# Kernel tuning notes

Hardware: AMD Instinct MI355X
Metric: run time of the kernel (lower is better)

The kernel has to match this reference:

```python
import jax, jax.numpy as jnp
import numpy as np

C_IN, C_OUT, N_FILTERS = 64, 256, 16
CK = C_IN * N_FILTERS  # 1024
B, N, E = 2, 10000, 120000


def setup_inputs() -> dict:
    key = jax.random.key(0)
    k1, k2, k3, k4, k5, k6, k7, k8 = jax.random.split(key, 8)
    node_feats = jax.random.normal(k1, (B, N, C_IN), dtype=jnp.float32)
    node_positions = jax.random.uniform(k2, (B, N, 3), dtype=jnp.float32)
    edge_src = jax.random.randint(k3, (E,), 0, N, dtype=jnp.int32)
    edge_dst = jax.random.randint(k4, (E,), 0, N, dtype=jnp.int32)
    # original skips self-connections inside the adjacency list (self term is added separately)
    edge_src = jnp.where(edge_src == edge_dst, (edge_src + 1) % N, edge_src)
    W_dir = jax.random.normal(k5, (CK, 3), dtype=jnp.float32) * 0.05
    b_dir = jax.random.normal(k6, (CK,), dtype=jnp.float32) * 0.05
    W_feat = jax.random.normal(k7, (C_OUT, CK), dtype=jnp.float32) * 0.05
    b_feat = jax.random.normal(k8, (C_OUT,), dtype=jnp.float32) * 0.05
    return {"node_feats": node_feats, "node_positions": node_positions,
            "edge_src": edge_src, "edge_dst": edge_dst,
            "W_dir": W_dir, "b_dir": b_dir, "W_feat": W_feat, "b_feat": b_feat}


def reference(node_feats, node_positions, edge_src, edge_dst, W_dir, b_dir, W_feat, b_feat):
    n = node_feats.shape[1]
    # stacked features: node_feats repeated n_filters times along channels -> [B,N,CK]
    stacked = jnp.tile(node_feats, (1, 1, N_FILTERS))
    # per-edge direction: pos_other - pos_this  (this = dst node being aggregated into)
    d = node_positions[:, edge_src] - node_positions[:, edge_dst]  # [B,E,3]
    aff = jax.nn.relu(jnp.einsum('bed,kd->bek', d, W_dir) + b_dir)  # [B,E,CK]
    msg = stacked[:, edge_src] * aff                                 # [B,E,CK]
    agg = jax.vmap(lambda m: jax.ops.segment_sum(m, edge_dst, num_segments=n))(msg)  # [B,N,CK]
    # self contribution: direction = 0 -> relu(b_dir), gated own features
    agg = agg + stacked * jax.nn.relu(b_dir)
    out = jax.nn.relu(jnp.einsum('bnk,ok->bno', agg, W_feat) + b_feat)  # [B,N,c_out]
    return out
```

## Files before the change

kernel.cpp:

```cpp
#include <hip/hip_runtime.h>
#include <hip/hip_bf16.h>
#include <cstdint>
#include <cstddef>

constexpr int BATCH = 2;
constexpr int C_IN  = 64;
constexpr int CK    = 1024;
constexpr int C_OUT = 256;

using bf16x8 = __attribute__((ext_vector_type(8))) short;
using f32x4  = __attribute__((ext_vector_type(4))) float;

#define GLOAD_LDS16(g, s) \
    __builtin_amdgcn_global_load_lds((const __attribute__((address_space(1))) void*)(g), \
                                     (__attribute__((address_space(3))) void*)(s), 16, 0, 0)

__global__ void hist_kernel(const int* __restrict__ dst, int* __restrict__ counts, int E) {
    int e = blockIdx.x * blockDim.x + threadIdx.x;
    if (e < E) atomicAdd(&counts[dst[e]], 1);
}

__global__ __launch_bounds__(1024)
void scan_kernel(const int* __restrict__ counts, int* __restrict__ offsets, int n) {
    __shared__ int wsum[16];
    __shared__ int carry_s;
    const int t = threadIdx.x;
    const int lane = t & 63;
    const int w = t >> 6;
    if (t == 0) carry_s = 0;
    __syncthreads();
    const int nch = (n + 1023) >> 10;
    for (int c = 0; c < nch; ++c) {
        const int idx = (c << 10) + t;
        const int v = (idx < n) ? counts[idx] : 0;
        int x = v;
        #pragma unroll
        for (int off = 1; off < 64; off <<= 1) {
            int y = __shfl_up(x, off, 64);
            if (lane >= off) x += y;
        }
        if (lane == 63) wsum[w] = x;
        __syncthreads();
        int wpre = 0, total = 0;
        #pragma unroll
        for (int i = 0; i < 16; ++i) {
            const int s = wsum[i];
            if (i < w) wpre += s;
            total += s;
        }
        const int carry = carry_s;
        if (idx < n) offsets[idx] = carry + wpre + (x - v);
        __syncthreads();
        if (t == 0) carry_s = carry + total;
    }
    if (t == 0) offsets[n] = carry_s;
}

__global__ void scatter_kernel(const int* __restrict__ dst, const int* __restrict__ src,
                               const int* __restrict__ offsets,
                               int* __restrict__ cursors, int* __restrict__ sorted_src, int E) {
    int e = blockIdx.x * blockDim.x + threadIdx.x;
    if (e < E) {
        const int d = dst[e];
        const int p = atomicAdd(&cursors[d], 1);
        sorted_src[offsets[d] + p] = src[e];
    }
}

__global__ __launch_bounds__(256)
void agg_kernel(const float* __restrict__ feats, const float* __restrict__ pos,
                const int* __restrict__ sorted_src, const int* __restrict__ offsets,
                const float* __restrict__ W_dir, const float* __restrict__ b_dir,
                __hip_bfloat16* __restrict__ agg, int N) {
    const int n = blockIdx.x;
    const int b = blockIdx.y;
    const int t = threadIdx.x;
    const int c0 = (2 * t) & 63;
    const float* posb   = pos   + (size_t)b * N * 3;
    const float* featsb = feats + (size_t)b * N * C_IN;

    const float px = posb[n * 3 + 0];
    const float py = posb[n * 3 + 1];
    const float pz = posb[n * 3 + 2];

    float wx[4], wy[4], wz[4], bb[4];
    #pragma unroll
    for (int u = 0; u < 4; ++u) {
        const int k = 2 * t + 512 * (u >> 1) + (u & 1);
        wx[u] = W_dir[k * 3 + 0];
        wy[u] = W_dir[k * 3 + 1];
        wz[u] = W_dir[k * 3 + 2];
        bb[u] = b_dir[k];
    }

    float acc[4] = {0.f, 0.f, 0.f, 0.f};
    const int beg = offsets[n];
    const int end = offsets[n + 1];
    for (int j = beg; j < end; ++j) {
        const int s = sorted_src[j];
        const float dx = posb[s * 3 + 0] - px;
        const float dy = posb[s * 3 + 1] - py;
        const float dz = posb[s * 3 + 2] - pz;
        const float2 f = *reinterpret_cast<const float2*>(featsb + (size_t)s * C_IN + c0);
        #pragma unroll
        for (int u = 0; u < 4; ++u) {
            const float a = fmaxf(fmaf(dx, wx[u], fmaf(dy, wy[u], fmaf(dz, wz[u], bb[u]))), 0.f);
            acc[u] += ((u & 1) ? f.y : f.x) * a;
        }
    }
    const float2 fs = *reinterpret_cast<const float2*>(featsb + (size_t)n * C_IN + c0);
    #pragma unroll
    for (int u = 0; u < 4; ++u) acc[u] += ((u & 1) ? fs.y : fs.x) * fmaxf(bb[u], 0.f);

    __hip_bfloat16* dst = agg + (size_t)(b * (size_t)N + n) * CK;
    __hip_bfloat162 v01, v23;
    v01.x = __float2bfloat16(acc[0]); v01.y = __float2bfloat16(acc[1]);
    v23.x = __float2bfloat16(acc[2]); v23.y = __float2bfloat16(acc[3]);
    *reinterpret_cast<__hip_bfloat162*>(dst + 2 * t)       = v01;
    *reinterpret_cast<__hip_bfloat162*>(dst + 2 * t + 512) = v23;
}

__global__ __launch_bounds__(256)
void cvtw_kernel(const float* __restrict__ in, __hip_bfloat16* __restrict__ out) {
    const int i = (blockIdx.x * 256 + threadIdx.x) * 4;
    const float4 v = *reinterpret_cast<const float4*>(in + i);
    __hip_bfloat162 a, b;
    a.x = __float2bfloat16(v.x); a.y = __float2bfloat16(v.y);
    b.x = __float2bfloat16(v.z); b.y = __float2bfloat16(v.w);
    *reinterpret_cast<__hip_bfloat162*>(out + i)     = a;
    *reinterpret_cast<__hip_bfloat162*>(out + i + 2) = b;
}

__global__ __launch_bounds__(256)
void gemm_kernel(const __hip_bfloat16* __restrict__ agg, const __hip_bfloat16* __restrict__ W,
                 const float* __restrict__ bf, float* __restrict__ out, int M) {
    __shared__ __hip_bfloat16 As[128 * 64];
    __shared__ __hip_bfloat16 Bs[128 * 64];
    const int t    = threadIdx.x;
    const int lane = t & 63;
    const int w    = t >> 6;
    const int q    = lane & 15;
    const int h    = lane >> 4;
    const int r0   = blockIdx.x * 128;
    const int c0   = blockIdx.y * 128;

    const int lrow   = lane >> 3;
    const int kschunk = (lane & 7) ^ lrow;

    f32x4 acc[4][4];
    #pragma unroll
    for (int mi = 0; mi < 4; ++mi)
        #pragma unroll
        for (int nj = 0; nj < 4; ++nj)
            #pragma unroll
            for (int r = 0; r < 4; ++r) acc[mi][nj][r] = 0.f;

    for (int k0 = 0; k0 < CK; k0 += 64) {
        #pragma unroll
        for (int i2 = 0; i2 < 4; ++i2) {
            const int seg = i2 * 4 + w;
            const int row = seg * 8 + lrow;
            const __hip_bfloat16* gA = agg + (size_t)(r0 + row) * CK + k0 + 8 * kschunk;
            const __hip_bfloat16* gB = W   + (size_t)(c0 + row) * CK + k0 + 8 * kschunk;
            GLOAD_LDS16(gA, As + seg * 512);
            GLOAD_LDS16(gB, Bs + seg * 512);
        }
        __syncthreads();

        #pragma unroll
        for (int kk = 0; kk < 2; ++kk) {
            bf16x8 af[4], bfr[4];
            #pragma unroll
            for (int mi = 0; mi < 4; ++mi) {
                const int row = (w >> 1) * 64 + mi * 16 + q;
                const int ch  = (kk * 4 + h) ^ (row & 7);
                af[mi] = *reinterpret_cast<const bf16x8*>(As + row * 64 + ch * 8);
            }
            #pragma unroll
            for (int nj = 0; nj < 4; ++nj) {
                const int row = (w & 1) * 64 + nj * 16 + q;
                const int ch  = (kk * 4 + h) ^ (row & 7);
                bfr[nj] = *reinterpret_cast<const bf16x8*>(Bs + row * 64 + ch * 8);
            }
            #pragma unroll
            for (int mi = 0; mi < 4; ++mi)
                #pragma unroll
                for (int nj = 0; nj < 4; ++nj)
                    acc[mi][nj] = __builtin_amdgcn_mfma_f32_16x16x32_bf16(
                        af[mi], bfr[nj], acc[mi][nj], 0, 0, 0);
        }
        __syncthreads();
    }

    #pragma unroll
    for (int mi = 0; mi < 4; ++mi) {
        #pragma unroll
        for (int nj = 0; nj < 4; ++nj) {
            const int col  = c0 + (w & 1) * 64 + nj * 16 + q;
            const float bias = bf[col];
            #pragma unroll
            for (int r = 0; r < 4; ++r) {
                const int row = r0 + (w >> 1) * 64 + mi * 16 + h * 4 + r;
                if (row < M)
                    out[(size_t)row * C_OUT + col] = fmaxf(acc[mi][nj][r] + bias, 0.f);
            }
        }
    }
}

extern "C" void kernel_launch(void* const* d_in, const int* in_sizes, int n_in,
                              void* d_out, int out_size, void* d_ws, size_t ws_size,
                              hipStream_t stream) {
    const float* feats  = (const float*)d_in[0];
    const float* pos    = (const float*)d_in[1];
    const int*   esrc   = (const int*)d_in[2];
    const int*   edst   = (const int*)d_in[3];
    const float* W_dir  = (const float*)d_in[4];
    const float* b_dir  = (const float*)d_in[5];
    const float* W_feat = (const float*)d_in[6];
    const float* b_feat = (const float*)d_in[7];
    float* out = (float*)d_out;

    const int N = in_sizes[1] / (BATCH * 3);
    const int E = in_sizes[2];
    const int M = BATCH * N;
    const int MBLK = (M + 127) / 128;
    const int M_pad = MBLK * 128;

    char* ws = (char*)d_ws;
    size_t off = 0;
    auto alignup = [&](size_t a) { off = (off + a - 1) & ~(a - 1); };

    __hip_bfloat16* agg = (__hip_bfloat16*)(ws + off); off += (size_t)M_pad * CK * sizeof(__hip_bfloat16);
    alignup(256);
    __hip_bfloat16* Wb  = (__hip_bfloat16*)(ws + off); off += (size_t)C_OUT * CK * sizeof(__hip_bfloat16);
    alignup(256);
    int* counts  = (int*)(ws + off); off += (size_t)N * sizeof(int);
    int* cursors = (int*)(ws + off); off += (size_t)N * sizeof(int);
    alignup(256);
    int* offsets = (int*)(ws + off); off += (size_t)(N + 1) * sizeof(int);
    alignup(256);
    int* sorted_src = (int*)(ws + off); off += (size_t)E * sizeof(int);

    hipMemsetAsync(counts, 0, (size_t)2 * N * sizeof(int), stream);
    hist_kernel<<<dim3((E + 255) / 256), dim3(256), 0, stream>>>(edst, counts, E);
    scan_kernel<<<dim3(1), dim3(1024), 0, stream>>>(counts, offsets, N);
    scatter_kernel<<<dim3((E + 255) / 256), dim3(256), 0, stream>>>(edst, esrc, offsets, cursors, sorted_src, E);
    cvtw_kernel<<<dim3(C_OUT * CK / 1024), dim3(256), 0, stream>>>(W_feat, Wb);
    agg_kernel<<<dim3(N, BATCH), dim3(256), 0, stream>>>(feats, pos, sorted_src, offsets,
                                                         W_dir, b_dir, agg, N);
    gemm_kernel<<<dim3(MBLK, C_OUT / 128), dim3(256), 0, stream>>>(agg, Wb, b_feat, out, M);
}
```

Baseline: 194.6 us.

## Merge batches per node block with LDS-staged neighbour features, shrink GEMM tiles

The aggregation kernel now handles both batch elements in one block per node. It stages neighbour indices, direction vectors and feature rows in shared memory in chunks of 32 edges, so the CSR indices and direction weights are loaded once and reused across batches. Direction weights are pre-packed into float4 by a fused prep kernel that also converts W_feat. The GEMM tile drops from 128x128 to 64x64 to launch more blocks for better occupancy, at the cost of less data reuse per tile and extra syncthreads in the aggregation loop.

```diff
diff --git a/kernel.cpp b/kernel.cpp
--- a/kernel.cpp
+++ b/kernel.cpp
@@ -7,6 +7,7 @@
 constexpr int C_IN  = 64;
 constexpr int CK    = 1024;
 constexpr int C_OUT = 256;
+constexpr int CHUNK = 32;
 
 using bf16x8 = __attribute__((ext_vector_type(8))) short;
 using f32x4  = __attribute__((ext_vector_type(4))) float;
@@ -68,96 +69,129 @@
 }
 
 __global__ __launch_bounds__(256)
-void agg_kernel(const float* __restrict__ feats, const float* __restrict__ pos,
-                const int* __restrict__ sorted_src, const int* __restrict__ offsets,
-                const float* __restrict__ W_dir, const float* __restrict__ b_dir,
-                __hip_bfloat16* __restrict__ agg, int N) {
-    const int n = blockIdx.x;
-    const int b = blockIdx.y;
-    const int t = threadIdx.x;
-    const int c0 = (2 * t) & 63;
-    const float* posb   = pos   + (size_t)b * N * 3;
-    const float* featsb = feats + (size_t)b * N * C_IN;
-
-    const float px = posb[n * 3 + 0];
-    const float py = posb[n * 3 + 1];
-    const float pz = posb[n * 3 + 2];
-
-    float wx[4], wy[4], wz[4], bb[4];
-    #pragma unroll
-    for (int u = 0; u < 4; ++u) {
-        const int k = 2 * t + 512 * (u >> 1) + (u & 1);
-        wx[u] = W_dir[k * 3 + 0];
-        wy[u] = W_dir[k * 3 + 1];
-        wz[u] = W_dir[k * 3 + 2];
-        bb[u] = b_dir[k];
-    }
-
-    float acc[4] = {0.f, 0.f, 0.f, 0.f};
-    const int beg = offsets[n];
-    const int end = offsets[n + 1];
-    for (int j = beg; j < end; ++j) {
-        const int s = sorted_src[j];
-        const float dx = posb[s * 3 + 0] - px;
-        const float dy = posb[s * 3 + 1] - py;
-        const float dz = posb[s * 3 + 2] - pz;
-        const float2 f = *reinterpret_cast<const float2*>(featsb + (size_t)s * C_IN + c0);
-        #pragma unroll
-        for (int u = 0; u < 4; ++u) {
-            const float a = fmaxf(fmaf(dx, wx[u], fmaf(dy, wy[u], fmaf(dz, wz[u], bb[u]))), 0.f);
-            acc[u] += ((u & 1) ? f.y : f.x) * a;
-        }
-    }
-    const float2 fs = *reinterpret_cast<const float2*>(featsb + (size_t)n * C_IN + c0);
-    #pragma unroll
-    for (int u = 0; u < 4; ++u) acc[u] += ((u & 1) ? fs.y : fs.x) * fmaxf(bb[u], 0.f);
-
-    __hip_bfloat16* dst = agg + (size_t)(b * (size_t)N + n) * CK;
-    __hip_bfloat162 v01, v23;
-    v01.x = __float2bfloat16(acc[0]); v01.y = __float2bfloat16(acc[1]);
-    v23.x = __float2bfloat16(acc[2]); v23.y = __float2bfloat16(acc[3]);
-    *reinterpret_cast<__hip_bfloat162*>(dst + 2 * t)       = v01;
-    *reinterpret_cast<__hip_bfloat162*>(dst + 2 * t + 512) = v23;
-}
-
-__global__ __launch_bounds__(256)
-void cvtw_kernel(const float* __restrict__ in, __hip_bfloat16* __restrict__ out) {
-    const int i = (blockIdx.x * 256 + threadIdx.x) * 4;
-    const float4 v = *reinterpret_cast<const float4*>(in + i);
+void prep_kernel(const float* __restrict__ Wf, __hip_bfloat16* __restrict__ Wb,
+                 const float* __restrict__ W_dir, const float* __restrict__ b_dir,
+                 float4* __restrict__ Wp) {
+    const int id = blockIdx.x * 256 + threadIdx.x;
+    const int i = id * 4;
+    const float4 v = *reinterpret_cast<const float4*>(Wf + i);
     __hip_bfloat162 a, b;
     a.x = __float2bfloat16(v.x); a.y = __float2bfloat16(v.y);
     b.x = __float2bfloat16(v.z); b.y = __float2bfloat16(v.w);
-    *reinterpret_cast<__hip_bfloat162*>(out + i)     = a;
-    *reinterpret_cast<__hip_bfloat162*>(out + i + 2) = b;
+    *reinterpret_cast<__hip_bfloat162*>(Wb + i)     = a;
+    *reinterpret_cast<__hip_bfloat162*>(Wb + i + 2) = b;
+    if (id < CK)
+        Wp[id] = make_float4(W_dir[id * 3 + 0], W_dir[id * 3 + 1], W_dir[id * 3 + 2], b_dir[id]);
+}
+
+__global__ __launch_bounds__(256)
+void agg_kernel(const float* __restrict__ feats, const float* __restrict__ pos,
+                const int* __restrict__ sorted_src, const int* __restrict__ offsets,
+                const float4* __restrict__ Wp,
+                __hip_bfloat16* __restrict__ agg, int N) {
+    __shared__ float  feats_s[BATCH][CHUNK][C_IN];
+    __shared__ float4 dir_s[BATCH][CHUNK];
+    __shared__ int    sh_s[CHUNK];
+
+    const int n = blockIdx.x;
+    const int t = threadIdx.x;
+    const int c0 = (2 * t) & 63;
+
+    float4 wv[4];
+    wv[0] = Wp[2 * t];       wv[1] = Wp[2 * t + 1];
+    wv[2] = Wp[2 * t + 512]; wv[3] = Wp[2 * t + 513];
+
+    float cx[BATCH], cy[BATCH], cz[BATCH];
+    #pragma unroll
+    for (int b = 0; b < BATCH; ++b) {
+        const float* pb = pos + ((size_t)b * N + n) * 3;
+        cx[b] = pb[0]; cy[b] = pb[1]; cz[b] = pb[2];
+    }
+
+    float acc[BATCH][4] = {};
+    const int beg = offsets[n], end = offsets[n + 1];
+
+    for (int j0 = beg; j0 < end; j0 += CHUNK) {
+        const int cnt = min(CHUNK, end - j0);
+        if (t < cnt) {
+            const int s = sorted_src[j0 + t];
+            sh_s[t] = s;
+            #pragma unroll
+            for (int b = 0; b < BATCH; ++b) {
+                const float* ps = pos + ((size_t)b * N + s) * 3;
+                dir_s[b][t] = make_float4(ps[0] - cx[b], ps[1] - cy[b], ps[2] - cz[b], 0.f);
+            }
+        }
+        __syncthreads();
+        #pragma unroll
+        for (int b = 0; b < BATCH; ++b) {
+            const float* fb = feats + (size_t)b * N * C_IN;
+            for (int idx = t; idx < cnt * C_IN; idx += 256) {
+                const int e = idx >> 6, ch = idx & 63;
+                feats_s[b][e][ch] = fb[(size_t)sh_s[e] * C_IN + ch];
+            }
+        }
+        __syncthreads();
+        #pragma unroll
+        for (int b = 0; b < BATCH; ++b) {
+            for (int j = 0; j < cnt; ++j) {
+                const float4 d = dir_s[b][j];
+                const float2 f = *reinterpret_cast<const float2*>(&feats_s[b][j][c0]);
+                #pragma unroll
+                for (int u = 0; u < 4; ++u) {
+                    const float a = fmaxf(fmaf(d.x, wv[u].x,
+                                         fmaf(d.y, wv[u].y,
+                                         fmaf(d.z, wv[u].z, wv[u].w))), 0.f);
+                    acc[b][u] += ((u & 1) ? f.y : f.x) * a;
+                }
+            }
+        }
+        __syncthreads();
+    }
+
+    #pragma unroll
+    for (int b = 0; b < BATCH; ++b) {
+        const float2 fs = *reinterpret_cast<const float2*>(
+            feats + ((size_t)b * N + n) * C_IN + c0);
+        #pragma unroll
+        for (int u = 0; u < 4; ++u)
+            acc[b][u] += ((u & 1) ? fs.y : fs.x) * fmaxf(wv[u].w, 0.f);
+        __hip_bfloat16* dst = agg + ((size_t)b * N + n) * CK;
+        __hip_bfloat162 v01, v23;
+        v01.x = __float2bfloat16(acc[b][0]); v01.y = __float2bfloat16(acc[b][1]);
+        v23.x = __float2bfloat16(acc[b][2]); v23.y = __float2bfloat16(acc[b][3]);
+        *reinterpret_cast<__hip_bfloat162*>(dst + 2 * t)       = v01;
+        *reinterpret_cast<__hip_bfloat162*>(dst + 2 * t + 512) = v23;
+    }
 }
 
 __global__ __launch_bounds__(256)
 void gemm_kernel(const __hip_bfloat16* __restrict__ agg, const __hip_bfloat16* __restrict__ W,
                  const float* __restrict__ bf, float* __restrict__ out, int M) {
-    __shared__ __hip_bfloat16 As[128 * 64];
-    __shared__ __hip_bfloat16 Bs[128 * 64];
+    __shared__ __hip_bfloat16 As[64 * 64];
+    __shared__ __hip_bfloat16 Bs[64 * 64];
     const int t    = threadIdx.x;
     const int lane = t & 63;
     const int w    = t >> 6;
     const int q    = lane & 15;
     const int h    = lane >> 4;
-    const int r0   = blockIdx.x * 128;
-    const int c0   = blockIdx.y * 128;
-
-    const int lrow   = lane >> 3;
+    const int r0   = blockIdx.x * 64;
+    const int c0   = blockIdx.y * 64;
+
+    const int lrow    = lane >> 3;
     const int kschunk = (lane & 7) ^ lrow;
 
-    f32x4 acc[4][4];
-    #pragma unroll
-    for (int mi = 0; mi < 4; ++mi)
-        #pragma unroll
-        for (int nj = 0; nj < 4; ++nj)
+    f32x4 acc[2][2];
+    #pragma unroll
+    for (int mi = 0; mi < 2; ++mi)
+        #pragma unroll
+        for (int nj = 0; nj < 2; ++nj)
             #pragma unroll
             for (int r = 0; r < 4; ++r) acc[mi][nj][r] = 0.f;
 
     for (int k0 = 0; k0 < CK; k0 += 64) {
         #pragma unroll
-        for (int i2 = 0; i2 < 4; ++i2) {
+        for (int i2 = 0; i2 < 2; ++i2) {
             const int seg = i2 * 4 + w;
             const int row = seg * 8 + lrow;
             const __hip_bfloat16* gA = agg + (size_t)(r0 + row) * CK + k0 + 8 * kschunk;
@@ -169,23 +203,23 @@
 
         #pragma unroll
         for (int kk = 0; kk < 2; ++kk) {
-            bf16x8 af[4], bfr[4];
-            #pragma unroll
-            for (int mi = 0; mi < 4; ++mi) {
-                const int row = (w >> 1) * 64 + mi * 16 + q;
+            bf16x8 af[2], bfr[2];
+            #pragma unroll
+            for (int mi = 0; mi < 2; ++mi) {
+                const int row = (w >> 1) * 32 + mi * 16 + q;
                 const int ch  = (kk * 4 + h) ^ (row & 7);
                 af[mi] = *reinterpret_cast<const bf16x8*>(As + row * 64 + ch * 8);
             }
             #pragma unroll
-            for (int nj = 0; nj < 4; ++nj) {
-                const int row = (w & 1) * 64 + nj * 16 + q;
+            for (int nj = 0; nj < 2; ++nj) {
+                const int row = (w & 1) * 32 + nj * 16 + q;
                 const int ch  = (kk * 4 + h) ^ (row & 7);
                 bfr[nj] = *reinterpret_cast<const bf16x8*>(Bs + row * 64 + ch * 8);
             }
             #pragma unroll
-            for (int mi = 0; mi < 4; ++mi)
+            for (int mi = 0; mi < 2; ++mi)
                 #pragma unroll
-                for (int nj = 0; nj < 4; ++nj)
+                for (int nj = 0; nj < 2; ++nj)
                     acc[mi][nj] = __builtin_amdgcn_mfma_f32_16x16x32_bf16(
                         af[mi], bfr[nj], acc[mi][nj], 0, 0, 0);
         }
@@ -193,14 +227,14 @@
     }
 
     #pragma unroll
-    for (int mi = 0; mi < 4; ++mi) {
-        #pragma unroll
-        for (int nj = 0; nj < 4; ++nj) {
-            const int col  = c0 + (w & 1) * 64 + nj * 16 + q;
+    for (int mi = 0; mi < 2; ++mi) {
+        #pragma unroll
+        for (int nj = 0; nj < 2; ++nj) {
+            const int col  = c0 + (w & 1) * 32 + nj * 16 + q;
             const float bias = bf[col];
             #pragma unroll
             for (int r = 0; r < 4; ++r) {
-                const int row = r0 + (w >> 1) * 64 + mi * 16 + h * 4 + r;
+                const int row = r0 + (w >> 1) * 32 + mi * 16 + h * 4 + r;
                 if (row < M)
                     out[(size_t)row * C_OUT + col] = fmaxf(acc[mi][nj][r] + bias, 0.f);
             }
@@ -224,8 +258,8 @@
     const int N = in_sizes[1] / (BATCH * 3);
     const int E = in_sizes[2];
     const int M = BATCH * N;
-    const int MBLK = (M + 127) / 128;
-    const int M_pad = MBLK * 128;
+    const int MBLK = (M + 63) / 64;
+    const int M_pad = MBLK * 64;
 
     char* ws = (char*)d_ws;
     size_t off = 0;
@@ -234,6 +268,8 @@
     __hip_bfloat16* agg = (__hip_bfloat16*)(ws + off); off += (size_t)M_pad * CK * sizeof(__hip_bfloat16);
     alignup(256);
     __hip_bfloat16* Wb  = (__hip_bfloat16*)(ws + off); off += (size_t)C_OUT * CK * sizeof(__hip_bfloat16);
+    alignup(256);
+    float4* Wp = (float4*)(ws + off); off += (size_t)CK * sizeof(float4);
     alignup(256);
     int* counts  = (int*)(ws + off); off += (size_t)N * sizeof(int);
     int* cursors = (int*)(ws + off); off += (size_t)N * sizeof(int);
@@ -246,8 +282,7 @@
     hist_kernel<<<dim3((E + 255) / 256), dim3(256), 0, stream>>>(edst, counts, E);
     scan_kernel<<<dim3(1), dim3(1024), 0, stream>>>(counts, offsets, N);
     scatter_kernel<<<dim3((E + 255) / 256), dim3(256), 0, stream>>>(edst, esrc, offsets, cursors, sorted_src, E);
-    cvtw_kernel<<<dim3(C_OUT * CK / 1024), dim3(256), 0, stream>>>(W_feat, Wb);
-    agg_kernel<<<dim3(N, BATCH), dim3(256), 0, stream>>>(feats, pos, sorted_src, offsets,
-                                                         W_dir, b_dir, agg, N);
-    gemm_kernel<<<dim3(MBLK, C_OUT / 128), dim3(256), 0, stream>>>(agg, Wb, b_feat, out, M);
-}
+    prep_kernel<<<dim3(C_OUT * CK / 1024), dim3(256), 0, stream>>>(W_feat, Wb, W_dir, b_dir, Wp);
+    agg_kernel<<<dim3(N), dim3(256), 0, stream>>>(feats, pos, sorted_src, offsets, Wp, agg, N);
+    gemm_kernel<<<dim3(MBLK, C_OUT / 64), dim3(256), 0, stream>>>(agg, Wb, b_feat, out, M);
+}
```

After: 177.1 us. 1.1x faster.
